# Kernel optimization log

Measured on AMD Instinct MI355X. Metric: run time of the kernel, lower is better.

Reference implementation:

```python
import jax, jax.numpy as jnp
import numpy as np


def setup_inputs() -> dict:
    key = jax.random.key(0)
    k1, k2, k3, k4 = jax.random.split(key, 4)
    B, T, C, D = 4, 2048, 1024, 128
    x = jax.random.normal(k1, (B, T, C), dtype=jnp.float32)
    # torch nn.Linear(in, out, bias=False) computes x @ W.T with W [out,in];
    # we store W as [in,out] so projection is x @ W (same math, transposed layout).
    Wq = jax.random.normal(k2, (C, D), dtype=jnp.float32) * (C ** -0.5)
    Wk = jax.random.normal(k3, (C, D), dtype=jnp.float32) * (C ** -0.5)
    Wv = jax.random.normal(k4, (C, D), dtype=jnp.float32) * (C ** -0.5)
    return {"x": x, "Wq": Wq, "Wk": Wk, "Wv": Wv}


def reference(x, Wq, Wk, Wv):
    B, T, C = x.shape
    D = Wq.shape[1]
    q = jnp.einsum("btc,cd->btd", x, Wq)
    k = jnp.einsum("btc,cd->btd", x, Wk)
    v = jnp.einsum("btc,cd->btd", x, Wv)
    scores = jnp.einsum("btd,bsd->bts", q, k) * (D ** -0.5)  # [B,T,T]
    causal = jnp.tril(jnp.ones((T, T), dtype=bool))
    scores = jnp.where(causal, scores, -jnp.inf)
    attn = jax.nn.softmax(scores, axis=-1)  # dropout_rate=0.0 -> identity
    return jnp.einsum("bts,bsd->btd", attn, v)
```

## Files before the change

kernel.cpp:

```cpp
#include <hip/hip_runtime.h>
#include <hip/hip_bf16.h>

typedef __attribute__((ext_vector_type(8))) short bf16x8;
typedef __attribute__((ext_vector_type(4))) short bf16x4;
typedef __attribute__((ext_vector_type(4))) float f32x4;

#define Tq 2048
#define Cq 1024
#define Dq 128

typedef const __attribute__((address_space(1))) void* gas_t;
typedef __attribute__((address_space(3))) void* las_t;

__device__ __forceinline__ short f2bf(float f) {
  unsigned u = __float_as_uint(f);
  u += 0x7fffu + ((u >> 16) & 1u);
  return (short)(u >> 16);
}
__device__ __forceinline__ float bf2f(short s) {
  return __uint_as_float(((unsigned)(unsigned short)s) << 16);
}
__device__ __forceinline__ float exp2a(float x) {
  float r;
  asm("v_exp_f32 %0, %1" : "=v"(r) : "v"(x));
  return r;
}
__device__ __forceinline__ int qi_of_slot(int s) {
  int o = s >> 3, k = s & 7;
  return o == 0 ? 31 - k : o == 1 ? 16 + k : o == 2 ? 15 - k : k;
}

__global__ __launch_bounds__(256) void pack_w_kernel(const float* __restrict__ Wq_,
                                                     const float* __restrict__ Wk_,
                                                     const float* __restrict__ Wv_,
                                                     short* __restrict__ wt) {
  int tid = blockIdx.x * 256 + threadIdx.x;
  int y   = tid >> 14;
  int idx = tid & 16383;
  int kg  = idx >> 7;
  int n   = idx & 127;
  const float* W = (y == 0) ? Wq_ : (y == 1 ? Wk_ : Wv_);
  float scale = (y == 0) ? 0.12751744f : 1.0f;
  bf16x8 o;
  #pragma unroll
  for (int j = 0; j < 8; ++j) o[j] = f2bf(W[(size_t)(kg * 8 + j) * Dq + n] * scale);
  *reinterpret_cast<bf16x8*>(wt + (size_t)y * 131072 + (size_t)n * 1024 + kg * 8) = o;
}

__global__ __launch_bounds__(256) void qkv_gemm_kernel(const float* __restrict__ x,
                                                       const short* __restrict__ wt,
                                                       short* __restrict__ qb,
                                                       short* __restrict__ kb2,
                                                       short* __restrict__ vt) {
  __shared__ float As[2][32][64];
  __shared__ short Bs[2][128][64];
  int y  = blockIdx.y;
  int bm = blockIdx.x;
  int w  = threadIdx.x >> 6, l = threadIdx.x & 63;
  int r  = l & 15, h = l >> 4;
  const short* wy = wt + (size_t)y * 131072;

  auto stage = [&](int t, int bi) {
    int k0 = t * 64;
    #pragma unroll
    for (int i = 0; i < 6; ++i) {
      int ii = w * 6 + i;
      if (ii < 8) {
        int row = ii * 4 + (l >> 4);
        int g   = l & 15;
        int sg  = (g & 8) | ((g & 7) ^ (row & 7));
        __builtin_amdgcn_global_load_lds(
            (gas_t)(x + (size_t)(bm * 32 + row) * Cq + k0 + sg * 4),
            (las_t)(&As[bi][ii * 4][0]), 16, 0, 0);
      } else {
        int jj  = ii - 8;
        int row = jj * 8 + (l >> 3);
        int sc  = ((l & 7) ^ (row & 7)) * 8;
        __builtin_amdgcn_global_load_lds(
            (gas_t)(wy + (size_t)row * Cq + k0 + sc),
            (las_t)(&Bs[bi][jj * 8][0]), 16, 0, 0);
      }
    }
  };

  f32x4 acc[2][2] = {};
  stage(0, 0);
  int cur = 0;
  for (int t = 0; t < 16; ++t, cur ^= 1) {
    stage(t + 1 < 16 ? t + 1 : t, cur ^ 1);
    asm volatile("s_waitcnt vmcnt(6)" ::: "memory");
    __builtin_amdgcn_s_barrier();
    __builtin_amdgcn_sched_barrier(0);
    bf16x8 af[2][2], bf[2][2];
    #pragma unroll
    for (int mi = 0; mi < 2; ++mi)
      #pragma unroll
      for (int kt = 0; kt < 2; ++kt) {
        int row = mi * 16 + r;
        int g0  = kt * 8 + h * 2;
        int s0  = (g0 & 8) | ((g0 & 7) ^ (row & 7));
        int g1  = g0 + 1;
        int s1  = (g1 & 8) | ((g1 & 7) ^ (row & 7));
        f32x4 fa = *reinterpret_cast<const f32x4*>(&As[cur][row][s0 * 4]);
        f32x4 fb = *reinterpret_cast<const f32x4*>(&As[cur][row][s1 * 4]);
        union { bf16x8 v; unsigned u[4]; } cv;
        asm("v_cvt_pk_bf16_f32 %0, %1, %2" : "=v"(cv.u[0]) : "v"(fa[0]), "v"(fa[1]));
        asm("v_cvt_pk_bf16_f32 %0, %1, %2" : "=v"(cv.u[1]) : "v"(fa[2]), "v"(fa[3]));
        asm("v_cvt_pk_bf16_f32 %0, %1, %2" : "=v"(cv.u[2]) : "v"(fb[0]), "v"(fb[1]));
        asm("v_cvt_pk_bf16_f32 %0, %1, %2" : "=v"(cv.u[3]) : "v"(fb[2]), "v"(fb[3]));
        af[mi][kt] = cv.v;
      }
    #pragma unroll
    for (int ni = 0; ni < 2; ++ni)
      #pragma unroll
      for (int kt = 0; kt < 2; ++kt) {
        int row = w * 32 + ni * 16 + r;
        bf[ni][kt] = *reinterpret_cast<const bf16x8*>(
            &Bs[cur][row][(kt * 32 + h * 8) ^ ((row & 7) << 3)]);
      }
    #pragma unroll
    for (int kt = 0; kt < 2; ++kt)
      #pragma unroll
      for (int mi = 0; mi < 2; ++mi)
        #pragma unroll
        for (int ni = 0; ni < 2; ++ni)
          acc[mi][ni] = __builtin_amdgcn_mfma_f32_16x16x32_bf16(af[mi][kt], bf[ni][kt], acc[mi][ni], 0, 0, 0);
    __builtin_amdgcn_sched_barrier(0);
    __builtin_amdgcn_s_barrier();
  }

  #pragma unroll
  for (int mi = 0; mi < 2; ++mi) {
    #pragma unroll
    for (int ni = 0; ni < 2; ++ni) {
      #pragma unroll
      for (int reg = 0; reg < 4; ++reg) {
        int m = bm * 32 + mi * 16 + h * 4 + reg;
        int n = w * 32 + ni * 16 + r;
        short s = f2bf(acc[mi][ni][reg]);
        if (y == 0)      qb[(size_t)m * Dq + n] = s;
        else if (y == 1) kb2[(size_t)m * Dq + n] = s;
        else {
          int bb = m >> 11, t2 = m & 2047;
          vt[((size_t)bb * Dq + n) * Tq + t2] = s;
        }
      }
    }
  }
}

__global__ __launch_bounds__(256, 4) void attn_kernel(const short* __restrict__ qb,
                                                      const short* __restrict__ kb2,
                                                      const short* __restrict__ vtb,
                                                      short* __restrict__ pacc,
                                                      float* __restrict__ pml) {
  __shared__ struct {
    short kb[2][32][128];
    short vb[2][128][32];
  } sm;

  int bid = blockIdx.x;
  int qi  = qi_of_slot(bid >> 5);
  int b   = (bid >> 3) & 3;
  int c   = bid & 7;
  int tid = threadIdx.x;
  int w   = tid >> 6, l = tid & 63;
  int r   = l & 15, h = l >> 4;

  int ntall = 2 * qi + 2;
  int clen  = (ntall + 7) >> 3;
  int tbeg  = c * clen;
  int tend  = ntall < tbeg + clen ? ntall : tbeg + clen;
  if (tbeg >= tend) return;

  int qw = qi * 64 + w * 16;
  const short* kbB = kb2 + (size_t)b * Tq * Dq;
  const short* vtB = vtb + (size_t)b * Dq * Tq;

  bf16x8 aq[4];
  size_t qbase = ((size_t)b * Tq + qw + r) * Dq;
  #pragma unroll
  for (int kt = 0; kt < 4; ++kt)
    aq[kt] = *reinterpret_cast<const bf16x8*>(qb + qbase + kt * 32 + h * 8);

  f32x4 acc[8] = {};
  float lrun = 0.0f;

  {
    auto stage = [&](int it, int bi) {
      int kv0 = it * 32;
      #pragma unroll
      for (int i2 = 0; i2 < 2; ++i2) {
        int i = w * 2 + i2;
        int row = i * 4 + (l >> 4);
        int sc  = ((l & 15) * 8) ^ ((row & 7) << 3);
        __builtin_amdgcn_global_load_lds(
            (gas_t)(kbB + (size_t)(kv0 + row) * Dq + sc),
            (las_t)(&sm.kb[bi][i * 4][0]), 16, 0, 0);
      }
      #pragma unroll
      for (int i2 = 0; i2 < 2; ++i2) {
        int i = w * 2 + i2;
        int row = i * 16 + (l >> 2);
        int sc  = ((l & 3) * 8) ^ ((row & 3) << 3);
        __builtin_amdgcn_global_load_lds(
            (gas_t)(vtB + (size_t)row * Tq + kv0 + sc),
            (las_t)(&sm.vb[bi][i * 16][0]), 16, 0, 0);
      }
    };

    stage(tbeg, 0);
    int cur = 0;
    for (int t = tbeg; t < tend; ++t, cur ^= 1) {
      stage(t + 1 < tend ? t + 1 : t, cur ^ 1);
      asm volatile("s_waitcnt vmcnt(4)" ::: "memory");
      __builtin_amdgcn_s_barrier();
      __builtin_amdgcn_sched_barrier(0);

      int kv0 = t * 32;
      bf16x8 kf[8];
      #pragma unroll
      for (int nt = 0; nt < 2; ++nt)
        #pragma unroll
        for (int kt = 0; kt < 4; ++kt) {
          int row = nt * 16 + r;
          kf[nt * 4 + kt] = *reinterpret_cast<const bf16x8*>(
              &sm.kb[cur][row][(kt * 32 + h * 8) ^ ((row & 7) << 3)]);
        }
      __builtin_amdgcn_sched_barrier(0);
      f32x4 s[2] = {};
      __builtin_amdgcn_s_setprio(1);
      #pragma unroll
      for (int nt = 0; nt < 2; ++nt)
        #pragma unroll
        for (int kt = 0; kt < 4; ++kt)
          s[nt] = __builtin_amdgcn_mfma_f32_16x16x32_bf16(
              kf[nt * 4 + kt], aq[kt], s[nt], 0, 0, 0);
      __builtin_amdgcn_s_setprio(0);

      bf16x8 vf[8];
      #pragma unroll
      for (int dt = 0; dt < 8; ++dt) {
        int row = dt * 16 + r;
        vf[dt] = *reinterpret_cast<const bf16x8*>(
            &sm.vb[cur][row][(h * 8) ^ ((row & 3) << 3)]);
      }

      if (kv0 + 31 > qw) {
        #pragma unroll
        for (int nt = 0; nt < 2; ++nt)
          #pragma unroll
          for (int reg = 0; reg < 4; ++reg)
            if (kv0 + nt * 16 + h * 4 + reg > qw + r) s[nt][reg] = -1e30f;
      }

      float p[2][4];
      #pragma unroll
      for (int nt = 0; nt < 2; ++nt)
        #pragma unroll
        for (int reg = 0; reg < 4; ++reg)
          p[nt][reg] = exp2a(s[nt][reg]);
      lrun += ((p[0][0] + p[0][1]) + (p[0][2] + p[0][3])) +
              ((p[1][0] + p[1][1]) + (p[1][2] + p[1][3]));

      unsigned wA0, wB0, wA1, wB1;
      asm("v_cvt_pk_bf16_f32 %0, %1, %2" : "=v"(wA0) : "v"(p[0][0]), "v"(p[0][1]));
      asm("v_cvt_pk_bf16_f32 %0, %1, %2" : "=v"(wB0) : "v"(p[0][2]), "v"(p[0][3]));
      asm("v_cvt_pk_bf16_f32 %0, %1, %2" : "=v"(wA1) : "v"(p[1][0]), "v"(p[1][1]));
      asm("v_cvt_pk_bf16_f32 %0, %1, %2" : "=v"(wB1) : "v"(p[1][2]), "v"(p[1][3]));
      int a0 = (((h & 1) << 5) + r) << 2;
      int a1 = a0 + 64;
      unsigned yA0  = __builtin_amdgcn_ds_bpermute(a0, wA0);
      unsigned yB0  = __builtin_amdgcn_ds_bpermute(a0, wB0);
      unsigned yA0b = __builtin_amdgcn_ds_bpermute(a1, wA0);
      unsigned yB0b = __builtin_amdgcn_ds_bpermute(a1, wB0);
      unsigned yA1  = __builtin_amdgcn_ds_bpermute(a0, wA1);
      unsigned yB1  = __builtin_amdgcn_ds_bpermute(a0, wB1);
      unsigned yA1b = __builtin_amdgcn_ds_bpermute(a1, wA1);
      unsigned yB1b = __builtin_amdgcn_ds_bpermute(a1, wB1);
      bool hi = h >= 2;
      union { unsigned u[4]; bf16x8 v; } pt;
      pt.u[0] = hi ? yA1  : yA0;
      pt.u[1] = hi ? yB1  : yB0;
      pt.u[2] = hi ? yA1b : yA0b;
      pt.u[3] = hi ? yB1b : yB0b;

      __builtin_amdgcn_s_setprio(1);
      #pragma unroll
      for (int dt = 0; dt < 8; ++dt)
        acc[dt] = __builtin_amdgcn_mfma_f32_16x16x32_bf16(vf[dt], pt.v, acc[dt], 0, 0, 0);
      __builtin_amdgcn_s_setprio(0);

      __builtin_amdgcn_sched_barrier(0);
      __builtin_amdgcn_s_barrier();
    }
  }

  float rs = lrun;
  rs += __shfl_xor(rs, 16);
  rs += __shfl_xor(rs, 32);
  if (h == 0) pml[(size_t)bid * 64 + w * 16 + r] = rs;
  size_t prow = (size_t)bid * 64 + w * 16 + r;
  #pragma unroll
  for (int dt = 0; dt < 8; ++dt) {
    bf16x4 o4;
    #pragma unroll
    for (int reg = 0; reg < 4; ++reg) o4[reg] = f2bf(acc[dt][reg]);
    *reinterpret_cast<bf16x4*>(&pacc[prow * 128 + dt * 16 + h * 4]) = o4;
  }
}

__global__ __launch_bounds__(256) void combine_kernel(const short* __restrict__ pacc,
                                                      const float* __restrict__ pml,
                                                      float* __restrict__ out) {
  int gid = blockIdx.x * 256 + threadIdx.x;
  int rg  = gid >> 5;
  int c4  = (gid & 31) * 4;
  int task = rg >> 6;
  int row  = rg & 63;
  int qi = qi_of_slot(task >> 2);
  int b  = task & 3;
  int bbase = task * 8;
  int ntall = 2 * qi + 2;
  int clen  = (ntall + 7) >> 3;
  float den = 0.0f;
  f32x4 num = {};
  #pragma unroll
  for (int cc = 0; cc < 8; ++cc) {
    if (cc * clen < ntall) {
      den += pml[(size_t)(bbase + cc) * 64 + row];
      bf16x4 a = *reinterpret_cast<const bf16x4*>(
          pacc + ((size_t)(bbase + cc) * 64 + row) * 128 + c4);
      #pragma unroll
      for (int j = 0; j < 4; ++j) num[j] += bf2f(a[j]);
    }
  }
  f32x4 o = num * (1.0f / den);
  *reinterpret_cast<f32x4*>(out + ((size_t)b * Tq + qi * 64 + row) * Dq + c4) = o;
}

extern "C" void kernel_launch(void* const* d_in, const int* in_sizes, int n_in,
                              void* d_out, int out_size, void* d_ws, size_t ws_size,
                              hipStream_t stream) {
  const float* x   = (const float*)d_in[0];
  const float* Wq_ = (const float*)d_in[1];
  const float* Wk_ = (const float*)d_in[2];
  const float* Wv_ = (const float*)d_in[3];
  float* out = (float*)d_out;
  char* ws = (char*)d_ws;
  short* wt   = (short*)(ws);
  short* qb   = (short*)(ws + 786432);
  short* kb   = (short*)(ws + 2883584);
  short* vt   = (short*)(ws + 4980736);
  float* pml  = (float*)(ws + 7077888);
  short* pacc = (short*)(ws + 7340032);

  hipLaunchKernelGGL(pack_w_kernel, dim3(192), dim3(256), 0, stream, Wq_, Wk_, Wv_, wt);
  hipLaunchKernelGGL(qkv_gemm_kernel, dim3(256, 3), dim3(256), 0, stream, x, wt, qb, kb, vt);
  hipLaunchKernelGGL(attn_kernel, dim3(1024), dim3(256), 0, stream, qb, kb, vt, pacc, pml);
  hipLaunchKernelGGL(combine_kernel, dim3(1024), dim3(256), 0, stream, pacc, pml, out);
}
```

Baseline: 50.32 us.

## Process two query row tiles per wave with 128-thread attention blocks

The attention kernel now launches 2 waves per block instead of 4, and each wave handles 32 query rows (two 16-row tiles) instead of 16. Each wave reuses its K and V fragments read from shared memory across both query tiles, which halves the LDS reads per query row and the number of waves that cooperate on staging. The tradeoff is higher register pressure (two sets of accumulators and scores), fewer waves per block to hide latency, and more staging loads per thread.

```diff
diff --git a/kernel.cpp b/kernel.cpp
--- a/kernel.cpp
+++ b/kernel.cpp
@@ -149,7 +149,7 @@
   }
 }
 
-__global__ __launch_bounds__(256, 4) void attn_kernel(const short* __restrict__ qb,
+__global__ __launch_bounds__(128, 3) void attn_kernel(const short* __restrict__ qb,
                                                       const short* __restrict__ kb2,
                                                       const short* __restrict__ vtb,
                                                       short* __restrict__ pacc,
@@ -173,25 +173,28 @@
   int tend  = ntall < tbeg + clen ? ntall : tbeg + clen;
   if (tbeg >= tend) return;
 
-  int qw = qi * 64 + w * 16;
+  int qw = qi * 64 + w * 32;
   const short* kbB = kb2 + (size_t)b * Tq * Dq;
   const short* vtB = vtb + (size_t)b * Dq * Tq;
 
-  bf16x8 aq[4];
-  size_t qbase = ((size_t)b * Tq + qw + r) * Dq;
-  #pragma unroll
-  for (int kt = 0; kt < 4; ++kt)
-    aq[kt] = *reinterpret_cast<const bf16x8*>(qb + qbase + kt * 32 + h * 8);
-
-  f32x4 acc[8] = {};
-  float lrun = 0.0f;
+  bf16x8 aq[2][4];
+  #pragma unroll
+  for (int j = 0; j < 2; ++j) {
+    size_t qbase = ((size_t)b * Tq + qw + j * 16 + r) * Dq;
+    #pragma unroll
+    for (int kt = 0; kt < 4; ++kt)
+      aq[j][kt] = *reinterpret_cast<const bf16x8*>(qb + qbase + kt * 32 + h * 8);
+  }
+
+  f32x4 acc[2][8] = {};
+  float lrun[2] = {0.0f, 0.0f};
 
   {
     auto stage = [&](int it, int bi) {
       int kv0 = it * 32;
       #pragma unroll
-      for (int i2 = 0; i2 < 2; ++i2) {
-        int i = w * 2 + i2;
+      for (int i2 = 0; i2 < 4; ++i2) {
+        int i = w * 4 + i2;
         int row = i * 4 + (l >> 4);
         int sc  = ((l & 15) * 8) ^ ((row & 7) << 3);
         __builtin_amdgcn_global_load_lds(
@@ -199,8 +202,8 @@
             (las_t)(&sm.kb[bi][i * 4][0]), 16, 0, 0);
       }
       #pragma unroll
-      for (int i2 = 0; i2 < 2; ++i2) {
-        int i = w * 2 + i2;
+      for (int i2 = 0; i2 < 4; ++i2) {
+        int i = w * 4 + i2;
         int row = i * 16 + (l >> 2);
         int sc  = ((l & 3) * 8) ^ ((row & 3) << 3);
         __builtin_amdgcn_global_load_lds(
@@ -213,7 +216,7 @@
     int cur = 0;
     for (int t = tbeg; t < tend; ++t, cur ^= 1) {
       stage(t + 1 < tend ? t + 1 : t, cur ^ 1);
-      asm volatile("s_waitcnt vmcnt(4)" ::: "memory");
+      asm volatile("s_waitcnt vmcnt(8)" ::: "memory");
       __builtin_amdgcn_s_barrier();
       __builtin_amdgcn_sched_barrier(0);
 
@@ -228,14 +231,16 @@
               &sm.kb[cur][row][(kt * 32 + h * 8) ^ ((row & 7) << 3)]);
         }
       __builtin_amdgcn_sched_barrier(0);
-      f32x4 s[2] = {};
+      f32x4 s[2][2] = {};
       __builtin_amdgcn_s_setprio(1);
       #pragma unroll
-      for (int nt = 0; nt < 2; ++nt)
-        #pragma unroll
-        for (int kt = 0; kt < 4; ++kt)
-          s[nt] = __builtin_amdgcn_mfma_f32_16x16x32_bf16(
-              kf[nt * 4 + kt], aq[kt], s[nt], 0, 0, 0);
+      for (int j = 0; j < 2; ++j)
+        #pragma unroll
+        for (int nt = 0; nt < 2; ++nt)
+          #pragma unroll
+          for (int kt = 0; kt < 4; ++kt)
+            s[j][nt] = __builtin_amdgcn_mfma_f32_16x16x32_bf16(
+                kf[nt * 4 + kt], aq[j][kt], s[j][nt], 0, 0, 0);
       __builtin_amdgcn_s_setprio(0);
 
       bf16x8 vf[8];
@@ -246,67 +251,74 @@
             &sm.vb[cur][row][(h * 8) ^ ((row & 3) << 3)]);
       }
 
-      if (kv0 + 31 > qw) {
+      #pragma unroll
+      for (int j = 0; j < 2; ++j) {
+        int qwj = qw + j * 16;
+        if (kv0 + 31 > qwj) {
+          #pragma unroll
+          for (int nt = 0; nt < 2; ++nt)
+            #pragma unroll
+            for (int reg = 0; reg < 4; ++reg)
+              if (kv0 + nt * 16 + h * 4 + reg > qwj + r) s[j][nt][reg] = -1e30f;
+        }
+
+        float p[2][4];
         #pragma unroll
         for (int nt = 0; nt < 2; ++nt)
           #pragma unroll
           for (int reg = 0; reg < 4; ++reg)
-            if (kv0 + nt * 16 + h * 4 + reg > qw + r) s[nt][reg] = -1e30f;
-      }
-
-      float p[2][4];
-      #pragma unroll
-      for (int nt = 0; nt < 2; ++nt)
-        #pragma unroll
-        for (int reg = 0; reg < 4; ++reg)
-          p[nt][reg] = exp2a(s[nt][reg]);
-      lrun += ((p[0][0] + p[0][1]) + (p[0][2] + p[0][3])) +
-              ((p[1][0] + p[1][1]) + (p[1][2] + p[1][3]));
-
-      unsigned wA0, wB0, wA1, wB1;
-      asm("v_cvt_pk_bf16_f32 %0, %1, %2" : "=v"(wA0) : "v"(p[0][0]), "v"(p[0][1]));
-      asm("v_cvt_pk_bf16_f32 %0, %1, %2" : "=v"(wB0) : "v"(p[0][2]), "v"(p[0][3]));
-      asm("v_cvt_pk_bf16_f32 %0, %1, %2" : "=v"(wA1) : "v"(p[1][0]), "v"(p[1][1]));
-      asm("v_cvt_pk_bf16_f32 %0, %1, %2" : "=v"(wB1) : "v"(p[1][2]), "v"(p[1][3]));
-      int a0 = (((h & 1) << 5) + r) << 2;
-      int a1 = a0 + 64;
-      unsigned yA0  = __builtin_amdgcn_ds_bpermute(a0, wA0);
-      unsigned yB0  = __builtin_amdgcn_ds_bpermute(a0, wB0);
-      unsigned yA0b = __builtin_amdgcn_ds_bpermute(a1, wA0);
-      unsigned yB0b = __builtin_amdgcn_ds_bpermute(a1, wB0);
-      unsigned yA1  = __builtin_amdgcn_ds_bpermute(a0, wA1);
-      unsigned yB1  = __builtin_amdgcn_ds_bpermute(a0, wB1);
-      unsigned yA1b = __builtin_amdgcn_ds_bpermute(a1, wA1);
-      unsigned yB1b = __builtin_amdgcn_ds_bpermute(a1, wB1);
-      bool hi = h >= 2;
-      union { unsigned u[4]; bf16x8 v; } pt;
-      pt.u[0] = hi ? yA1  : yA0;
-      pt.u[1] = hi ? yB1  : yB0;
-      pt.u[2] = hi ? yA1b : yA0b;
-      pt.u[3] = hi ? yB1b : yB0b;
-
-      __builtin_amdgcn_s_setprio(1);
-      #pragma unroll
-      for (int dt = 0; dt < 8; ++dt)
-        acc[dt] = __builtin_amdgcn_mfma_f32_16x16x32_bf16(vf[dt], pt.v, acc[dt], 0, 0, 0);
-      __builtin_amdgcn_s_setprio(0);
+            p[nt][reg] = exp2a(s[j][nt][reg]);
+        lrun[j] += ((p[0][0] + p[0][1]) + (p[0][2] + p[0][3])) +
+                   ((p[1][0] + p[1][1]) + (p[1][2] + p[1][3]));
+
+        unsigned wA0, wB0, wA1, wB1;
+        asm("v_cvt_pk_bf16_f32 %0, %1, %2" : "=v"(wA0) : "v"(p[0][0]), "v"(p[0][1]));
+        asm("v_cvt_pk_bf16_f32 %0, %1, %2" : "=v"(wB0) : "v"(p[0][2]), "v"(p[0][3]));
+        asm("v_cvt_pk_bf16_f32 %0, %1, %2" : "=v"(wA1) : "v"(p[1][0]), "v"(p[1][1]));
+        asm("v_cvt_pk_bf16_f32 %0, %1, %2" : "=v"(wB1) : "v"(p[1][2]), "v"(p[1][3]));
+        int a0 = (((h & 1) << 5) + r) << 2;
+        int a1 = a0 + 64;
+        unsigned yA0  = __builtin_amdgcn_ds_bpermute(a0, wA0);
+        unsigned yB0  = __builtin_amdgcn_ds_bpermute(a0, wB0);
+        unsigned yA0b = __builtin_amdgcn_ds_bpermute(a1, wA0);
+        unsigned yB0b = __builtin_amdgcn_ds_bpermute(a1, wB0);
+        unsigned yA1  = __builtin_amdgcn_ds_bpermute(a0, wA1);
+        unsigned yB1  = __builtin_amdgcn_ds_bpermute(a0, wB1);
+        unsigned yA1b = __builtin_amdgcn_ds_bpermute(a1, wA1);
+        unsigned yB1b = __builtin_amdgcn_ds_bpermute(a1, wB1);
+        bool hi = h >= 2;
+        union { unsigned u[4]; bf16x8 v; } pt;
+        pt.u[0] = hi ? yA1  : yA0;
+        pt.u[1] = hi ? yB1  : yB0;
+        pt.u[2] = hi ? yA1b : yA0b;
+        pt.u[3] = hi ? yB1b : yB0b;
+
+        __builtin_amdgcn_s_setprio(1);
+        #pragma unroll
+        for (int dt = 0; dt < 8; ++dt)
+          acc[j][dt] = __builtin_amdgcn_mfma_f32_16x16x32_bf16(vf[dt], pt.v, acc[j][dt], 0, 0, 0);
+        __builtin_amdgcn_s_setprio(0);
+      }
 
       __builtin_amdgcn_sched_barrier(0);
       __builtin_amdgcn_s_barrier();
     }
   }
 
-  float rs = lrun;
-  rs += __shfl_xor(rs, 16);
-  rs += __shfl_xor(rs, 32);
-  if (h == 0) pml[(size_t)bid * 64 + w * 16 + r] = rs;
-  size_t prow = (size_t)bid * 64 + w * 16 + r;
-  #pragma unroll
-  for (int dt = 0; dt < 8; ++dt) {
-    bf16x4 o4;
-    #pragma unroll
-    for (int reg = 0; reg < 4; ++reg) o4[reg] = f2bf(acc[dt][reg]);
-    *reinterpret_cast<bf16x4*>(&pacc[prow * 128 + dt * 16 + h * 4]) = o4;
+  #pragma unroll
+  for (int j = 0; j < 2; ++j) {
+    float rs = lrun[j];
+    rs += __shfl_xor(rs, 16);
+    rs += __shfl_xor(rs, 32);
+    if (h == 0) pml[(size_t)bid * 64 + w * 32 + j * 16 + r] = rs;
+    size_t prow = (size_t)bid * 64 + w * 32 + j * 16 + r;
+    #pragma unroll
+    for (int dt = 0; dt < 8; ++dt) {
+      bf16x4 o4;
+      #pragma unroll
+      for (int reg = 0; reg < 4; ++reg) o4[reg] = f2bf(acc[j][dt][reg]);
+      *reinterpret_cast<bf16x4*>(&pacc[prow * 128 + dt * 16 + h * 4]) = o4;
+    }
   }
 }
 
@@ -357,6 +369,6 @@
 
   hipLaunchKernelGGL(pack_w_kernel, dim3(192), dim3(256), 0, stream, Wq_, Wk_, Wv_, wt);
   hipLaunchKernelGGL(qkv_gemm_kernel, dim3(256, 3), dim3(256), 0, stream, x, wt, qb, kb, vt);
-  hipLaunchKernelGGL(attn_kernel, dim3(1024), dim3(256), 0, stream, qb, kb, vt, pacc, pml);
+  hipLaunchKernelGGL(attn_kernel, dim3(1024), dim3(128), 0, stream, qb, kb, vt, pacc, pml);
   hipLaunchKernelGGL(combine_kernel, dim3(1024), dim3(256), 0, stream, pacc, pml, out);
 }
```

Result: slower. 66.54 us (+32.2%).
